# Kernel optimization log

Measured on AMD Instinct MI355X. Metric: run time of the kernel, lower is better.

The kernel has to match this reference:

```python
import jax, jax.numpy as jnp
import numpy as np

SCALE = 64.0  # quantization scale (step = 1/SCALE), also threshold clamp floor


def setup_inputs() -> dict:
    key = jax.random.key(0)
    x = jax.random.normal(key, (32, 2048, 512), dtype=jnp.float32)  # [B, C, T]
    threshold = jnp.array([0.1], dtype=jnp.float32)  # shared learnable threshold
    return {"x": x, "threshold": threshold}


def _delta_scan(x, thr):
    """Delta differential encoding with residual carry (cum_error=False).

    delta[t] = x[t] - x[t-1] + r[t-1]
    y[t]     = delta[t] if |delta[t]| >= thr else 0
    r[t]     = delta[t] - y[t]
    """
    xt = jnp.moveaxis(x, -1, 0)  # [T, B, C]
    zeros = jnp.zeros_like(xt[0])
    def step(carry, xi):
        pre, res = carry
        delta = xi - pre + res
        y = jnp.where(jnp.abs(delta) >= thr, delta, jnp.zeros_like(delta))
        return (xi, delta - y), y
    _, ys = jax.lax.scan(step, (zeros, zeros), xt)
    return jnp.moveaxis(ys, 0, -1)  # [B, C, T]


def reference(x, threshold):
    # threshold clamp to [1/scale, inf)
    thr = jnp.maximum(threshold, 1.0 / SCALE)
    y = _delta_scan(x, thr)
    # quantize(output, step=1/scale, mode=FLOOR)
    return jnp.floor(y * SCALE) / SCALE
```

## Files before the change

### kernel.cpp

```cpp
#include <hip/hip_runtime.h>


#define T_LEN 512

constexpr int BLOCK   = 256;
constexpr int WAVE    = 64;
constexpr int CV      = 16;
constexpr int NCHUNK  = T_LEN / (CV * 4);

__global__ __launch_bounds__(BLOCK, 1) void delta_scan_kernel(
    const float* __restrict__ x,
    const float* __restrict__ thrp,
    float* __restrict__ out)
{
    __shared__ float4 lds[BLOCK / WAVE][WAVE * CV];

    const int tid  = threadIdx.x;
    const int wid  = tid >> 6;
    const int lane = tid & 63;
    float4* __restrict__ wlds = lds[wid];

    const int row   = blockIdx.x * BLOCK + tid;
    const int wrow0 = blockIdx.x * BLOCK + wid * WAVE;

    const float thr = fmaxf(thrp[0], 0.015625f);

    const float4* __restrict__ xv = reinterpret_cast<const float4*>(x);
    float4* __restrict__       ov = reinterpret_cast<float4*>(out);
    const size_t rbase = (size_t)row * (T_LEN / 4);

    float pre = 0.0f, res = 0.0f;
    float4 va[CV], vb[CV];

#pragma unroll
    for (int i = 0; i < CV; ++i) va[i] = xv[rbase + i];

#pragma unroll
    for (int c = 0; c < NCHUNK; ++c) {
        float4* cur = (c & 1) ? vb : va;
        float4* nxt = (c & 1) ? va : vb;

        if (c + 1 < NCHUNK) {
#pragma unroll
            for (int i = 0; i < CV; ++i) nxt[i] = xv[rbase + (c + 1) * CV + i];
        }

#pragma unroll
        for (int i = 0; i < CV; ++i) {
            float4 v = cur[i];
            float4 q;
            { float d=(v.x-pre)+res; bool b=fabsf(d)>=thr; float y=b?d:0.0f;
              res=b?0.0f:d; pre=v.x; q.x=floorf(y*64.0f)*0.015625f; }
            { float d=(v.y-pre)+res; bool b=fabsf(d)>=thr; float y=b?d:0.0f;
              res=b?0.0f:d; pre=v.y; q.y=floorf(y*64.0f)*0.015625f; }
            { float d=(v.z-pre)+res; bool b=fabsf(d)>=thr; float y=b?d:0.0f;
              res=b?0.0f:d; pre=v.z; q.z=floorf(y*64.0f)*0.015625f; }
            { float d=(v.w-pre)+res; bool b=fabsf(d)>=thr; float y=b?d:0.0f;
              res=b?0.0f:d; pre=v.w; q.w=floorf(y*64.0f)*0.015625f; }

            wlds[lane * CV + (i ^ (lane & 7))] = q;
        }

#pragma unroll
        for (int k = 0; k < 16; ++k) {
            const int rr = k * 4 + (lane >> 4);
            const int jj = lane & 15;
            const float4 t4 = wlds[rr * CV + (jj ^ (rr & 7))];
            ov[(size_t)(wrow0 + rr) * (T_LEN / 4) + c * CV + jj] = t4;
        }
    }
}

extern "C" void kernel_launch(void* const* d_in, const int* in_sizes, int n_in,
                              void* d_out, int out_size, void* d_ws, size_t ws_size,
                              hipStream_t stream)
{
    const float* x    = (const float*)d_in[0];
    const float* thrp = (const float*)d_in[1];
    float*       out  = (float*)d_out;

    const int rows = in_sizes[0] / T_LEN;
    const int grid = rows / BLOCK;

    delta_scan_kernel<<<grid, BLOCK, 0, stream>>>(x, thrp, out);
}
```

Baseline: 240.5 us.

## Triple-buffer global loads and double-buffer LDS transpose to overlap stores with compute

Register prefetching moves from two buffers to three, so loads are issued two chunks ahead. LDS staging is double-buffered and the coalesced stores for chunk c-1 are deferred until iteration c, so the next chunk's compute can overlap with draining the previous chunk. Compiler memory barriers are added to hold the load issue order in place. The cost is roughly 16 more float4 registers per thread (occupancy is already capped at one block per CU by the launch bounds) and twice the LDS. A cross-lane LDS read with no wave barrier is relied on, which is only safe within a single wave.

```diff
diff --git a/kernel.cpp b/kernel.cpp
--- a/kernel.cpp
+++ b/kernel.cpp
@@ -3,22 +3,21 @@
 
 #define T_LEN 512
 
-constexpr int BLOCK   = 256;
-constexpr int WAVE    = 64;
-constexpr int CV      = 16;
-constexpr int NCHUNK  = T_LEN / (CV * 4);
+constexpr int BLOCK  = 256;
+constexpr int WAVE   = 64;
+constexpr int CV     = 16;
+constexpr int NCHUNK = T_LEN / (CV * 4);
 
 __global__ __launch_bounds__(BLOCK, 1) void delta_scan_kernel(
     const float* __restrict__ x,
     const float* __restrict__ thrp,
     float* __restrict__ out)
 {
-    __shared__ float4 lds[BLOCK / WAVE][WAVE * CV];
+    __shared__ float4 lds[2][BLOCK / WAVE][WAVE * CV];
 
     const int tid  = threadIdx.x;
     const int wid  = tid >> 6;
     const int lane = tid & 63;
-    float4* __restrict__ wlds = lds[wid];
 
     const int row   = blockIdx.x * BLOCK + tid;
     const int wrow0 = blockIdx.x * BLOCK + wid * WAVE;
@@ -29,22 +28,38 @@
     float4* __restrict__       ov = reinterpret_cast<float4*>(out);
     const size_t rbase = (size_t)row * (T_LEN / 4);
 
+    float4 bA[CV], bB[CV], bC[CV];
     float pre = 0.0f, res = 0.0f;
-    float4 va[CV], vb[CV];
 
 #pragma unroll
-    for (int i = 0; i < CV; ++i) va[i] = xv[rbase + i];
+    for (int i = 0; i < CV; ++i) bA[i] = xv[rbase + i];
+#pragma unroll
+    for (int i = 0; i < CV; ++i) bB[i] = xv[rbase + CV + i];
+    asm volatile("" ::: "memory");
 
 #pragma unroll
     for (int c = 0; c < NCHUNK; ++c) {
-        float4* cur = (c & 1) ? vb : va;
-        float4* nxt = (c & 1) ? va : vb;
+        float4* cur = (c % 3 == 0) ? bA : ((c % 3 == 1) ? bB : bC);
+        float4* nx2 = ((c + 2) % 3 == 0) ? bA : (((c + 2) % 3 == 1) ? bB : bC);
 
-        if (c + 1 < NCHUNK) {
+        if (c + 2 < NCHUNK) {
 #pragma unroll
-            for (int i = 0; i < CV; ++i) nxt[i] = xv[rbase + (c + 1) * CV + i];
+            for (int i = 0; i < CV; ++i) nx2[i] = xv[rbase + (c + 2) * CV + i];
+            asm volatile("" ::: "memory");
         }
 
+        if (c > 0) {
+            const float4* pt = lds[(c - 1) & 1][wid];
+#pragma unroll
+            for (int k = 0; k < 16; ++k) {
+                const int rr = k * 4 + (lane >> 4);
+                const int jj = lane & 15;
+                const float4 t4 = pt[rr * CV + (jj ^ (rr & 7))];
+                ov[(size_t)(wrow0 + rr) * (T_LEN / 4) + (c - 1) * CV + jj] = t4;
+            }
+        }
+
+        float4* wt = lds[c & 1][wid];
 #pragma unroll
         for (int i = 0; i < CV; ++i) {
             float4 v = cur[i];
@@ -58,15 +73,18 @@
             { float d=(v.w-pre)+res; bool b=fabsf(d)>=thr; float y=b?d:0.0f;
               res=b?0.0f:d; pre=v.w; q.w=floorf(y*64.0f)*0.015625f; }
 
-            wlds[lane * CV + (i ^ (lane & 7))] = q;
+            wt[lane * CV + (i ^ (lane & 7))] = q;
         }
+    }
 
+    {
+        const float4* pt = lds[(NCHUNK - 1) & 1][wid];
 #pragma unroll
         for (int k = 0; k < 16; ++k) {
             const int rr = k * 4 + (lane >> 4);
             const int jj = lane & 15;
-            const float4 t4 = wlds[rr * CV + (jj ^ (rr & 7))];
-            ov[(size_t)(wrow0 + rr) * (T_LEN / 4) + c * CV + jj] = t4;
+            const float4 t4 = pt[rr * CV + (jj ^ (rr & 7))];
+            ov[(size_t)(wrow0 + rr) * (T_LEN / 4) + (NCHUNK - 1) * CV + jj] = t4;
         }
     }
 }
```

Result: no change. 239.7 us (-0.3%).

## Stage input through a 3-deep LDS ring via async global_load_lds

Applied to the files above, without the earlier changes.

Input chunks now go straight from global memory into a per-wave three-slot LDS ring with the global_load_lds builtin, instead of being double-buffered in registers. Loads are issued two chunks ahead and completion is tracked with an explicit s_waitcnt vmcnt. The chunk size drops from 16 to 8 float4 per row, and the output transpose buffer shrinks to match. The aim is deeper load overlap and lower register pressure. The cost is more chunk iterations, and correctness depends on a hand-counted vmcnt that assumes stores and loads share one in-order counter.

```diff
diff --git a/kernel.cpp b/kernel.cpp
--- a/kernel.cpp
+++ b/kernel.cpp
@@ -3,22 +3,25 @@
 
 #define T_LEN 512
 
-constexpr int BLOCK   = 256;
-constexpr int WAVE    = 64;
-constexpr int CV      = 16;
-constexpr int NCHUNK  = T_LEN / (CV * 4);
+constexpr int BLOCK  = 256;
+constexpr int WAVE   = 64;
+constexpr int CF4    = 8;
+constexpr int RPF4   = T_LEN / 4;
+constexpr int NCHUNK = RPF4 / CF4;
+constexpr int RING   = 3;
+constexpr int NWAVE  = BLOCK / WAVE;
 
 __global__ __launch_bounds__(BLOCK, 1) void delta_scan_kernel(
     const float* __restrict__ x,
     const float* __restrict__ thrp,
     float* __restrict__ out)
 {
-    __shared__ float4 lds[BLOCK / WAVE][WAVE * CV];
+    __shared__ float4 in_t[NWAVE][RING][CF4 * WAVE];
+    __shared__ float4 out_t[NWAVE][WAVE * CF4];
 
     const int tid  = threadIdx.x;
     const int wid  = tid >> 6;
     const int lane = tid & 63;
-    float4* __restrict__ wlds = lds[wid];
 
     const int row   = blockIdx.x * BLOCK + tid;
     const int wrow0 = blockIdx.x * BLOCK + wid * WAVE;
@@ -27,27 +30,35 @@
 
     const float4* __restrict__ xv = reinterpret_cast<const float4*>(x);
     float4* __restrict__       ov = reinterpret_cast<float4*>(out);
-    const size_t rbase = (size_t)row * (T_LEN / 4);
+    const size_t rb = (size_t)row * RPF4;
+
+    float4* const ot = out_t[wid];
+
+#define STAGE(cc)                                                         \
+    {                                                                     \
+        float4* dst = in_t[wid][(cc) % RING];                             \
+        _Pragma("unroll")                                                 \
+        for (int k = 0; k < CF4; ++k)                                     \
+            __builtin_amdgcn_global_load_lds(                             \
+                (const void*)&xv[rb + (size_t)(cc) * CF4 + k],            \
+                (void*)&dst[k * WAVE], 16, 0, 0);                         \
+    }
+
+    STAGE(0)
+    STAGE(1)
 
     float pre = 0.0f, res = 0.0f;
-    float4 va[CV], vb[CV];
-
-#pragma unroll
-    for (int i = 0; i < CV; ++i) va[i] = xv[rbase + i];
 
 #pragma unroll
     for (int c = 0; c < NCHUNK; ++c) {
-        float4* cur = (c & 1) ? vb : va;
-        float4* nxt = (c & 1) ? va : vb;
+        if (c + 2 < NCHUNK) STAGE(c + 2)
 
-        if (c + 1 < NCHUNK) {
+        asm volatile("s_waitcnt vmcnt(16)" ::: "memory");
+
+        const float4* src = in_t[wid][c % RING];
 #pragma unroll
-            for (int i = 0; i < CV; ++i) nxt[i] = xv[rbase + (c + 1) * CV + i];
-        }
-
-#pragma unroll
-        for (int i = 0; i < CV; ++i) {
-            float4 v = cur[i];
+        for (int i = 0; i < CF4; ++i) {
+            const float4 v = src[i * WAVE + lane];
             float4 q;
             { float d=(v.x-pre)+res; bool b=fabsf(d)>=thr; float y=b?d:0.0f;
               res=b?0.0f:d; pre=v.x; q.x=floorf(y*64.0f)*0.015625f; }
@@ -58,17 +69,18 @@
             { float d=(v.w-pre)+res; bool b=fabsf(d)>=thr; float y=b?d:0.0f;
               res=b?0.0f:d; pre=v.w; q.w=floorf(y*64.0f)*0.015625f; }
 
-            wlds[lane * CV + (i ^ (lane & 7))] = q;
+            ot[lane * CF4 + (i ^ (lane & 7))] = q;
         }
 
 #pragma unroll
-        for (int k = 0; k < 16; ++k) {
-            const int rr = k * 4 + (lane >> 4);
-            const int jj = lane & 15;
-            const float4 t4 = wlds[rr * CV + (jj ^ (rr & 7))];
-            ov[(size_t)(wrow0 + rr) * (T_LEN / 4) + c * CV + jj] = t4;
+        for (int k = 0; k < CF4; ++k) {
+            const int rr = k * 8 + (lane >> 3);
+            const int jj = lane & 7;
+            const float4 t4 = ot[rr * CF4 + (jj ^ (rr & 7))];
+            ov[(size_t)(wrow0 + rr) * RPF4 + c * CF4 + jj] = t4;
         }
     }
+#undef STAGE
 }
 
 extern "C" void kernel_launch(void* const* d_in, const int* in_sizes, int n_in,
```

After: 243.6 us. No clear change (+1.3%).

## Split time axis into segments with speculative scan and residual fix-up pass

Applied to the files above, without the earlier changes.

Each row's 512-step scan is split into 8 segments. Each segment is scanned in parallel assuming a zero incoming residual, and its final residual goes to workspace. A second kernel walks the segments per row, recomputing each segment's prefix with the true carried residual until it converges with the speculative trajectory, then overwrites those outputs. This gives many more threads for latency hiding, since the original had only 256 blocks of one row per thread. The cost is a second launch, extra workspace traffic and a serial fix-up pass that reads and writes scalars without coalescing.

```diff
diff --git a/kernel.cpp b/kernel.cpp
--- a/kernel.cpp
+++ b/kernel.cpp
@@ -3,71 +3,113 @@
 
 #define T_LEN 512
 
-constexpr int BLOCK   = 256;
-constexpr int WAVE    = 64;
-constexpr int CV      = 16;
-constexpr int NCHUNK  = T_LEN / (CV * 4);
+constexpr int SEGS   = 8;
+constexpr int SEGLEN = T_LEN / SEGS;
+constexpr int SEGF4  = SEGLEN / 4;
+constexpr int BLOCK1 = 256;
+constexpr int BLOCK2 = 256;
 
-__global__ __launch_bounds__(BLOCK, 1) void delta_scan_kernel(
+__global__ __launch_bounds__(BLOCK1, 4) void delta_seg_kernel(
     const float* __restrict__ x,
     const float* __restrict__ thrp,
-    float* __restrict__ out)
+    float* __restrict__ out,
+    float* __restrict__ res_ws)
 {
-    __shared__ float4 lds[BLOCK / WAVE][WAVE * CV];
+    __shared__ float4 tile[BLOCK1 / 64][64 * 8];
 
     const int tid  = threadIdx.x;
     const int wid  = tid >> 6;
     const int lane = tid & 63;
-    float4* __restrict__ wlds = lds[wid];
-
-    const int row   = blockIdx.x * BLOCK + tid;
-    const int wrow0 = blockIdx.x * BLOCK + wid * WAVE;
+    const int g    = blockIdx.x * BLOCK1 + tid;
+    const int row  = g >> 3;
+    const int s    = g & 7;
+    const int row0 = (blockIdx.x * BLOCK1 + wid * 64) >> 3;
 
     const float thr = fmaxf(thrp[0], 0.015625f);
 
+    const size_t base = (size_t)row * T_LEN + (size_t)s * SEGLEN;
     const float4* __restrict__ xv = reinterpret_cast<const float4*>(x);
     float4* __restrict__       ov = reinterpret_cast<float4*>(out);
-    const size_t rbase = (size_t)row * (T_LEN / 4);
 
-    float pre = 0.0f, res = 0.0f;
-    float4 va[CV], vb[CV];
+    float pre = 0.0f;
+    if (s != 0) pre = x[base - 1];
+    float res = 0.0f;
+
+    float4 v[SEGF4];
+#pragma unroll
+    for (int i = 0; i < SEGF4; ++i) v[i] = xv[(base >> 2) + i];
+
+    float4* const wt = tile[wid];
 
 #pragma unroll
-    for (int i = 0; i < CV; ++i) va[i] = xv[rbase + i];
-
+    for (int pass = 0; pass < 2; ++pass) {
+        float4 q[8];
 #pragma unroll
-    for (int c = 0; c < NCHUNK; ++c) {
-        float4* cur = (c & 1) ? vb : va;
-        float4* nxt = (c & 1) ? va : vb;
-
-        if (c + 1 < NCHUNK) {
-#pragma unroll
-            for (int i = 0; i < CV; ++i) nxt[i] = xv[rbase + (c + 1) * CV + i];
+        for (int i = 0; i < 8; ++i) {
+            const float4 vv = v[pass * 8 + i];
+            float4 qq;
+            { float d=(vv.x-pre)+res; bool b=fabsf(d)>=thr; float y=b?d:0.0f;
+              res=b?0.0f:d; pre=vv.x; qq.x=floorf(y*64.0f)*0.015625f; }
+            { float d=(vv.y-pre)+res; bool b=fabsf(d)>=thr; float y=b?d:0.0f;
+              res=b?0.0f:d; pre=vv.y; qq.y=floorf(y*64.0f)*0.015625f; }
+            { float d=(vv.z-pre)+res; bool b=fabsf(d)>=thr; float y=b?d:0.0f;
+              res=b?0.0f:d; pre=vv.z; qq.z=floorf(y*64.0f)*0.015625f; }
+            { float d=(vv.w-pre)+res; bool b=fabsf(d)>=thr; float y=b?d:0.0f;
+              res=b?0.0f:d; pre=vv.w; qq.w=floorf(y*64.0f)*0.015625f; }
+            q[i] = qq;
         }
 
 #pragma unroll
-        for (int i = 0; i < CV; ++i) {
-            float4 v = cur[i];
-            float4 q;
-            { float d=(v.x-pre)+res; bool b=fabsf(d)>=thr; float y=b?d:0.0f;
-              res=b?0.0f:d; pre=v.x; q.x=floorf(y*64.0f)*0.015625f; }
-            { float d=(v.y-pre)+res; bool b=fabsf(d)>=thr; float y=b?d:0.0f;
-              res=b?0.0f:d; pre=v.y; q.y=floorf(y*64.0f)*0.015625f; }
-            { float d=(v.z-pre)+res; bool b=fabsf(d)>=thr; float y=b?d:0.0f;
-              res=b?0.0f:d; pre=v.z; q.z=floorf(y*64.0f)*0.015625f; }
-            { float d=(v.w-pre)+res; bool b=fabsf(d)>=thr; float y=b?d:0.0f;
-              res=b?0.0f:d; pre=v.w; q.w=floorf(y*64.0f)*0.015625f; }
-
-            wlds[lane * CV + (i ^ (lane & 7))] = q;
-        }
+        for (int i = 0; i < 8; ++i)
+            wt[lane * 8 + (i ^ (lane & 7))] = q[i];
 
 #pragma unroll
-        for (int k = 0; k < 16; ++k) {
-            const int rr = k * 4 + (lane >> 4);
-            const int jj = lane & 15;
-            const float4 t4 = wlds[rr * CV + (jj ^ (rr & 7))];
-            ov[(size_t)(wrow0 + rr) * (T_LEN / 4) + c * CV + jj] = t4;
+        for (int k = 0; k < 8; ++k) {
+            const int S  = k * 8 + (lane >> 3);
+            const float4 t4 = wt[S * 8 + ((lane & 7) ^ (S & 7))];
+            ov[(size_t)(row0 + k) * (T_LEN / 4)
+               + (lane >> 3) * SEGF4 + pass * 8 + (lane & 7)] = t4;
         }
+    }
+
+    res_ws[g] = res;
+}
+
+__global__ __launch_bounds__(BLOCK2) void delta_fix_kernel(
+    const float* __restrict__ x,
+    const float* __restrict__ thrp,
+    float* __restrict__ out,
+    const float* __restrict__ res_ws)
+{
+    const int row = blockIdx.x * BLOCK2 + threadIdx.x;
+    const float thr = fmaxf(thrp[0], 0.015625f);
+
+    float res = res_ws[row * SEGS + 0];
+
+    for (int s = 1; s < SEGS; ++s) {
+        if (res == 0.0f) {
+            res = res_ws[row * SEGS + s];
+            continue;
+        }
+        const size_t base = (size_t)row * T_LEN + (size_t)s * SEGLEN;
+        float pre    = x[base - 1];
+        float res_tr = res;
+        float res_sp = 0.0f;
+        bool  conv   = false;
+        for (int t = 0; t < SEGLEN; ++t) {
+            const float xi  = x[base + t];
+            const float dtr = (xi - pre) + res_tr;
+            const float dsp = (xi - pre) + res_sp;
+            const bool  ftr = fabsf(dtr) >= thr;
+            const bool  fsp = fabsf(dsp) >= thr;
+            const float y   = ftr ? dtr : 0.0f;
+            out[base + t]   = floorf(y * 64.0f) * 0.015625f;
+            res_tr = ftr ? 0.0f : dtr;
+            res_sp = fsp ? 0.0f : dsp;
+            pre = xi;
+            if (ftr && fsp) { conv = true; break; }
+        }
+        res = conv ? res_ws[row * SEGS + s] : res_tr;
     }
 }
 
@@ -78,9 +120,12 @@
     const float* x    = (const float*)d_in[0];
     const float* thrp = (const float*)d_in[1];
     float*       out  = (float*)d_out;
+    float*       ws   = (float*)d_ws;
 
-    const int rows = in_sizes[0] / T_LEN;
-    const int grid = rows / BLOCK;
+    const int rows  = in_sizes[0] / T_LEN;
+    const int grid1 = rows * SEGS / BLOCK1;
+    const int grid2 = rows / BLOCK2;
 
-    delta_scan_kernel<<<grid, BLOCK, 0, stream>>>(x, thrp, out);
+    delta_seg_kernel<<<grid1, BLOCK1, 0, stream>>>(x, thrp, out, ws);
+    delta_fix_kernel<<<grid2, BLOCK2, 0, stream>>>(x, thrp, out, ws);
 }
```

After: 253.8 us. 5.5% more time.
